# Optimization experiments

Hardware: AMD Instinct MI355X
Metric: run time of the kernel (lower is better)

The kernel has to match this reference:

```python
import jax, jax.numpy as jnp
import numpy as np

EPS = 1e-8


def setup_inputs() -> dict:
    key = jax.random.key(0)
    ks = jax.random.split(key, 10)
    B, Cin, H, W = 16, 256, 64, 64
    D, C = 128, 32
    return {
        "f_curr": jax.random.normal(ks[0], (B, Cin, H, W), jnp.float32),
        "mu_prior": jax.random.normal(ks[1], (B, D, C), jnp.float32),
        "log_sigma_prior": jax.random.normal(ks[2], (B, D, C), jnp.float32),
        "pi_prior": jax.random.uniform(ks[3], (B, C), jnp.float32),
        "mu_post": jax.random.normal(ks[4], (B, D), jnp.float32),
        "log_sigma_post": jax.random.normal(ks[5], (B, D), jnp.float32),
        "noise_cluster": jax.random.normal(ks[6], (B, D), jnp.float32),
        "noise_z": jax.random.normal(ks[7], (B, D), jnp.float32),
        "proj_W": jax.random.normal(ks[8], (Cin, Cin + D), jnp.float32) * 0.02,
        "proj_b": jax.random.normal(ks[9], (Cin,), jnp.float32) * 0.02,
    }


def reference(f_curr, mu_prior, log_sigma_prior, pi_prior, mu_post,
              log_sigma_post, noise_cluster, noise_z, proj_W, proj_b):
    sg = jax.lax.stop_gradient

    # ---- _cluster_sampler (all stats detached in the original) ----
    mu_p, ls_p = sg(mu_post), sg(log_sigma_post)          # [B, D]
    mu_pr, ls_pr = sg(mu_prior), sg(log_sigma_prior)      # [B, D, C]
    z_post = mu_p + jnp.exp(ls_p) * noise_cluster          # Normal(mu, exp(ls)).sample()
    sigma_pr = jnp.exp(ls_pr)
    # Normal log_prob of z_post[:, :, None] under each cluster -> [B, D, C]
    log_probs = (-ls_pr - 0.5 * jnp.log(2.0 * jnp.pi)
                 - (z_post[:, :, None] - mu_pr) ** 2 / (2.0 * sigma_pr ** 2))
    log_prob_c = jnp.sum(log_probs, axis=1)                # [B, C]
    pi_post = jax.nn.softmax(log_prob_c, axis=1)           # [B, C]

    # ---- z_c = Normal(mu_post, exp(ls)+eps).sample()  (no grad: .sample()) ----
    z_c = sg(mu_post + (jnp.exp(log_sigma_post) + EPS) * noise_z)  # [B, D]

    # ---- _f_combine: concat + 1x1 conv, computed as split matmuls ----
    Cin = f_curr.shape[1]
    Wf, Wz = proj_W[:, :Cin], proj_W[:, Cin:]              # [Cin,Cin], [Cin,D]
    bias = jnp.einsum('bd,od->bo', z_c, Wz) + proj_b       # spatially-constant part
    f_out = jnp.einsum('bchw,oc->bohw', f_curr, Wf) + bias[:, :, None, None]

    # ---- _kld ----
    mu_post_e = mu_post[:, :, None]                        # [B, D, 1]
    ls_post_e = log_sigma_post[:, :, None]
    sigma_prior = jnp.exp(log_sigma_prior)
    sigma_post = jnp.exp(ls_post_e)
    kl_g = (log_sigma_prior - ls_post_e
            + (sigma_post ** 2 + (mu_post_e - mu_prior) ** 2)
            / (2.0 * sigma_prior ** 2 + EPS) - 0.5)
    kl_g = jnp.sum(kl_g, axis=1)                           # [B, C]
    kl_g_weighted = jnp.sum(pi_post * kl_g, axis=1)        # [B]
    kl_cat = jnp.sum(pi_post * (jnp.log(pi_post + EPS) - jnp.log(pi_prior + EPS)), axis=1)  # [B]
    kl_std = jnp.sum(-ls_post_e + 0.5 * (jnp.exp(2.0 * ls_post_e) + mu_post_e ** 2) - 0.5,
                     axis=1)                               # [B, 1]
    # NOTE: original torch code broadcasts [B] + [B,1] -> [B,B] before mean; replicated here.
    kld = jnp.mean((kl_g_weighted + kl_cat) + kl_std)

    return f_out, kld
```

## Files before the change

kernel.cpp:

```cpp
#include <hip/hip_runtime.h>
#include <math.h>

#define EPS_F 1e-8f

typedef __attribute__((ext_vector_type(8))) short bf16x8;
typedef __attribute__((ext_vector_type(4))) float f32x4;

__device__ inline short f2bf(float f) {
    union { float f; unsigned u; } v; v.f = f;
    unsigned r = (v.u + 0x7fffu + ((v.u >> 16) & 1u)) >> 16;
    return (short)r;
}

__global__ __launch_bounds__(256) void prelim_kernel(
    const float* __restrict__ mu_prior,
    const float* __restrict__ ls_prior,
    const float* __restrict__ pi_prior,
    const float* __restrict__ mu_post,
    const float* __restrict__ ls_post,
    const float* __restrict__ noise_c,
    const float* __restrict__ noise_z,
    const float* __restrict__ projW,
    const float* __restrict__ projb,
    float* __restrict__ ws_bias,
    float* __restrict__ kld_out)
{
    const int b = blockIdx.x;
    const int t = threadIdx.x;

    __shared__ float s_zpost[128];
    __shared__ float s_zc[128];
    __shared__ float s_mu[128];
    __shared__ float s_e2[128];
    __shared__ float s_lsp[128];
    __shared__ float s_kstd[128];
    __shared__ float s_p1[8][32];
    __shared__ float s_p2[8][32];

    if (t < 128) {
        const float mu = mu_post[b * 128 + t];
        const float ls = ls_post[b * 128 + t];
        const float el = __expf(ls);
        s_zpost[t] = mu + el * noise_c[b * 128 + t];
        s_zc[t]    = mu + (el + EPS_F) * noise_z[b * 128 + t];
        s_mu[t]    = mu;
        s_e2[t]    = el * el;
        s_lsp[t]   = ls;
        s_kstd[t]  = -ls + 0.5f * (el * el + mu * mu) - 0.5f;
    }
    __syncthreads();

    {
        const int c = t & 31;
        const int g = t >> 5;
        const float* mpB = mu_prior + b * 4096;
        const float* lpB = ls_prior + b * 4096;
        float lp = 0.f, kg = 0.f;
#pragma unroll 4
        for (int j = 0; j < 16; ++j) {
            const int d = g * 16 + j;
            const float mpr  = mpB[d * 32 + c];
            const float lpr  = lpB[d * 32 + c];
            const float inv2 = 0.5f * __expf(-2.f * lpr);
            const float zd   = s_zpost[d] - mpr;
            lp += -lpr - 0.91893853320467274f - zd * zd * inv2;
            const float dm   = s_mu[d] - mpr;
            const float e2pr = __expf(2.f * lpr);
            kg += lpr - s_lsp[d]
                + (s_e2[d] + dm * dm) * __builtin_amdgcn_rcpf(2.f * e2pr + EPS_F)
                - 0.5f;
        }
        s_p1[g][c] = lp;
        s_p2[g][c] = kg;
    }
    __syncthreads();

    if (t < 64) {
        const int c = t & 31;
        float lp = 0.f, kg = 0.f;
#pragma unroll
        for (int g = 0; g < 8; ++g) { lp += s_p1[g][c]; kg += s_p2[g][c]; }
        float ks = s_kstd[c] + s_kstd[c + 32] + s_kstd[c + 64] + s_kstd[c + 96];
        const float pp = pi_prior[b * 32 + c];

        float m = lp;
#pragma unroll
        for (int o = 16; o; o >>= 1) m = fmaxf(m, __shfl_xor(m, o, 32));
        const float e = __expf(lp - m);
        float den = e;
#pragma unroll
        for (int o = 16; o; o >>= 1) den += __shfl_xor(den, o, 32);
        const float pi = e * __builtin_amdgcn_rcpf(den);
        float tot = pi * kg + pi * (__logf(pi + EPS_F) - __logf(pp + EPS_F));
#pragma unroll
        for (int o = 16; o; o >>= 1) tot += __shfl_xor(tot, o, 32);
#pragma unroll
        for (int o = 16; o; o >>= 1) ks += __shfl_xor(ks, o, 32);
        if (t == 0) atomicAdd(kld_out, (tot + ks) * 0.0625f);
    }

    {
        const int o = t;
        const float4* wrow = (const float4*)(projW + o * 384 + 256);
        float sum = projb[o];
#pragma unroll 8
        for (int j = 0; j < 32; ++j) {
            const float4 w = wrow[j];
            sum += s_zc[4 * j + 0] * w.x + s_zc[4 * j + 1] * w.y +
                   s_zc[4 * j + 2] * w.z + s_zc[4 * j + 3] * w.w;
        }
        ws_bias[b * 256 + o] = sum;
    }
}

__global__ __launch_bounds__(512, 2) void gemm_kernel(
    const float* __restrict__ F,
    const float* __restrict__ W,
    const float* __restrict__ bias,
    float* __restrict__ O)
{
    const int nT = blockIdx.x;
    const int b  = blockIdx.y;

    __shared__ short A_lds[4][256][8];
    __shared__ short B_lds[4][128][8];
    __shared__ float s_bias[256];

    const int tid  = threadIdx.x;
    const int lane = tid & 63;
    const int wave = tid >> 6;
    const int wm = wave & 3;
    const int wn = wave >> 2;

    const float* Fb = F + (size_t)b * 256 * 4096 + (size_t)nT * 128;

    const int sbn = tid & 127;
    const int sbk = tid >> 7;
    const int sao = tid >> 1;
    const int sak = (tid & 1) * 2;

    if (tid < 256) s_bias[tid] = bias[b * 256 + tid];

    const float* bptr = Fb + (size_t)(sbk * 8) * 4096 + sbn;
    const float* aptr = W + sao * 384 + sak * 8;

    float fb[8];
    float4 fa0, fa1, fa2, fa3;

#pragma unroll
    for (int i = 0; i < 8; ++i) fb[i] = bptr[(size_t)i * 4096];
    fa0 = *(const float4*)(aptr);
    fa1 = *(const float4*)(aptr + 4);
    fa2 = *(const float4*)(aptr + 8);
    fa3 = *(const float4*)(aptr + 12);

    f32x4 acc[4][4];
#pragma unroll
    for (int i = 0; i < 4; ++i)
#pragma unroll
        for (int j = 0; j < 4; ++j) acc[i][j] = (f32x4){0.f, 0.f, 0.f, 0.f};

    const int kg = lane >> 4;
    const int lm = lane & 15;

    for (int kc = 0; kc < 8; ++kc) {
        bf16x8 vb, va0, va1;
#pragma unroll
        for (int i = 0; i < 8; ++i) vb[i] = f2bf(fb[i]);
        va0[0] = f2bf(fa0.x); va0[1] = f2bf(fa0.y); va0[2] = f2bf(fa0.z); va0[3] = f2bf(fa0.w);
        va0[4] = f2bf(fa1.x); va0[5] = f2bf(fa1.y); va0[6] = f2bf(fa1.z); va0[7] = f2bf(fa1.w);
        va1[0] = f2bf(fa2.x); va1[1] = f2bf(fa2.y); va1[2] = f2bf(fa2.z); va1[3] = f2bf(fa2.w);
        va1[4] = f2bf(fa3.x); va1[5] = f2bf(fa3.y); va1[6] = f2bf(fa3.z); va1[7] = f2bf(fa3.w);

        __syncthreads();
        *(bf16x8*)&B_lds[sbk][sbn][0]     = vb;
        *(bf16x8*)&A_lds[sak][sao][0]     = va0;
        *(bf16x8*)&A_lds[sak + 1][sao][0] = va1;
        __syncthreads();

        if (kc < 7) {
            const float* bp = bptr + (size_t)(kc + 1) * 32 * 4096;
#pragma unroll
            for (int i = 0; i < 8; ++i) fb[i] = bp[(size_t)i * 4096];
            const float* ap = aptr + (kc + 1) * 32;
            fa0 = *(const float4*)(ap);
            fa1 = *(const float4*)(ap + 4);
            fa2 = *(const float4*)(ap + 8);
            fa3 = *(const float4*)(ap + 12);
        }

        bf16x8 aF[4], bF[4];
#pragma unroll
        for (int mt = 0; mt < 4; ++mt)
            aF[mt] = *(const bf16x8*)&A_lds[kg][wm * 64 + mt * 16 + lm][0];
#pragma unroll
        for (int nt = 0; nt < 4; ++nt)
            bF[nt] = *(const bf16x8*)&B_lds[kg][wn * 64 + nt * 16 + lm][0];

#pragma unroll
        for (int mt = 0; mt < 4; ++mt)
#pragma unroll
            for (int nt = 0; nt < 4; ++nt)
                acc[mt][nt] = __builtin_amdgcn_mfma_f32_16x16x32_bf16(
                    aF[mt], bF[nt], acc[mt][nt], 0, 0, 0);
    }

    float* Ob = O + (size_t)b * 256 * 4096;
    const int rbase = wm * 64 + (lane >> 4) * 4;
    const int cbase = nT * 128 + wn * 64 + (lane & 15);
#pragma unroll
    for (int mt = 0; mt < 4; ++mt) {
#pragma unroll
        for (int r = 0; r < 4; ++r) {
            const int row = rbase + mt * 16 + r;
            const float bb = s_bias[row];
            float* orow = Ob + (size_t)row * 4096 + cbase;
#pragma unroll
            for (int nt = 0; nt < 4; ++nt)
                orow[nt * 16] = acc[mt][nt][r] + bb;
        }
    }
}

extern "C" void kernel_launch(void* const* d_in, const int* in_sizes, int n_in,
                              void* d_out, int out_size, void* d_ws, size_t ws_size,
                              hipStream_t stream) {
    const float* f_curr   = (const float*)d_in[0];
    const float* mu_prior = (const float*)d_in[1];
    const float* ls_prior = (const float*)d_in[2];
    const float* pi_prior = (const float*)d_in[3];
    const float* mu_post  = (const float*)d_in[4];
    const float* ls_post  = (const float*)d_in[5];
    const float* noise_c  = (const float*)d_in[6];
    const float* noise_z  = (const float*)d_in[7];
    const float* projW    = (const float*)d_in[8];
    const float* projb    = (const float*)d_in[9];

    float* out = (float*)d_out;
    float* ws  = (float*)d_ws;
    float* ws_bias = ws;

    float* kld_out = out + 16777216;
    hipMemsetAsync(kld_out, 0, sizeof(float), stream);

    prelim_kernel<<<16, 256, 0, stream>>>(mu_prior, ls_prior, pi_prior, mu_post,
                                          ls_post, noise_c, noise_z, projW, projb,
                                          ws_bias, kld_out);
    gemm_kernel<<<dim3(32, 16), 512, 0, stream>>>(f_curr, projW, ws_bias, out);
}
```

Baseline: 156.3 us.

## Split GEMM output channels across two blocks with 256-thread tiles

The GEMM grid gains an output-channel tile dimension, so each block computes a 128x128 output tile with 4 waves instead of a 256x128 tile with 8 waves. This doubles the block count (1024 blocks) to improve occupancy and load balance across CUs. Each thread now stages 16 F values per k-chunk. The cost is that every F tile is read twice from global memory, once per output-channel half, and per-block staging work rises.

```diff
diff --git a/kernel.cpp b/kernel.cpp
--- a/kernel.cpp
+++ b/kernel.cpp
@@ -113,42 +113,43 @@
     }
 }
 
-__global__ __launch_bounds__(512, 2) void gemm_kernel(
+__global__ __launch_bounds__(256) void gemm_kernel(
     const float* __restrict__ F,
     const float* __restrict__ W,
     const float* __restrict__ bias,
     float* __restrict__ O)
 {
     const int nT = blockIdx.x;
-    const int b  = blockIdx.y;
-
-    __shared__ short A_lds[4][256][8];
+    const int oT = blockIdx.y;
+    const int b  = blockIdx.z;
+
+    __shared__ short A_lds[4][128][8];
     __shared__ short B_lds[4][128][8];
-    __shared__ float s_bias[256];
+    __shared__ float s_bias[128];
 
     const int tid  = threadIdx.x;
     const int lane = tid & 63;
     const int wave = tid >> 6;
-    const int wm = wave & 3;
-    const int wn = wave >> 2;
+    const int wm = wave & 1;
+    const int wn = wave >> 1;
 
     const float* Fb = F + (size_t)b * 256 * 4096 + (size_t)nT * 128;
 
-    const int sbn = tid & 127;
-    const int sbk = tid >> 7;
-    const int sao = tid >> 1;
-    const int sak = (tid & 1) * 2;
-
-    if (tid < 256) s_bias[tid] = bias[b * 256 + tid];
-
-    const float* bptr = Fb + (size_t)(sbk * 8) * 4096 + sbn;
-    const float* aptr = W + sao * 384 + sak * 8;
-
-    float fb[8];
+    const int sbn  = tid & 127;
+    const int sbkg = (tid >> 7) * 2;
+    const int sao  = tid >> 1;
+    const int sakg = (tid & 1) * 2;
+
+    if (tid < 128) s_bias[tid] = bias[b * 256 + oT * 128 + tid];
+
+    const float* bptr = Fb + (size_t)(sbkg * 8) * 4096 + sbn;
+    const float* aptr = W + (size_t)(oT * 128 + sao) * 384 + sakg * 8;
+
+    float fb[16];
     float4 fa0, fa1, fa2, fa3;
 
 #pragma unroll
-    for (int i = 0; i < 8; ++i) fb[i] = bptr[(size_t)i * 4096];
+    for (int i = 0; i < 16; ++i) fb[i] = bptr[(size_t)i * 4096];
     fa0 = *(const float4*)(aptr);
     fa1 = *(const float4*)(aptr + 4);
     fa2 = *(const float4*)(aptr + 8);
@@ -164,24 +165,27 @@
     const int lm = lane & 15;
 
     for (int kc = 0; kc < 8; ++kc) {
-        bf16x8 vb, va0, va1;
-#pragma unroll
-        for (int i = 0; i < 8; ++i) vb[i] = f2bf(fb[i]);
+        bf16x8 vb0, vb1, va0, va1;
+#pragma unroll
+        for (int i = 0; i < 8; ++i) vb0[i] = f2bf(fb[i]);
+#pragma unroll
+        for (int i = 0; i < 8; ++i) vb1[i] = f2bf(fb[8 + i]);
         va0[0] = f2bf(fa0.x); va0[1] = f2bf(fa0.y); va0[2] = f2bf(fa0.z); va0[3] = f2bf(fa0.w);
         va0[4] = f2bf(fa1.x); va0[5] = f2bf(fa1.y); va0[6] = f2bf(fa1.z); va0[7] = f2bf(fa1.w);
         va1[0] = f2bf(fa2.x); va1[1] = f2bf(fa2.y); va1[2] = f2bf(fa2.z); va1[3] = f2bf(fa2.w);
         va1[4] = f2bf(fa3.x); va1[5] = f2bf(fa3.y); va1[6] = f2bf(fa3.z); va1[7] = f2bf(fa3.w);
 
         __syncthreads();
-        *(bf16x8*)&B_lds[sbk][sbn][0]     = vb;
-        *(bf16x8*)&A_lds[sak][sao][0]     = va0;
-        *(bf16x8*)&A_lds[sak + 1][sao][0] = va1;
+        *(bf16x8*)&B_lds[sbkg][sbn][0]      = vb0;
+        *(bf16x8*)&B_lds[sbkg + 1][sbn][0]  = vb1;
+        *(bf16x8*)&A_lds[sakg][sao][0]      = va0;
+        *(bf16x8*)&A_lds[sakg + 1][sao][0]  = va1;
         __syncthreads();
 
         if (kc < 7) {
             const float* bp = bptr + (size_t)(kc + 1) * 32 * 4096;
 #pragma unroll
-            for (int i = 0; i < 8; ++i) fb[i] = bp[(size_t)i * 4096];
+            for (int i = 0; i < 16; ++i) fb[i] = bp[(size_t)i * 4096];
             const float* ap = aptr + (kc + 1) * 32;
             fa0 = *(const float4*)(ap);
             fa1 = *(const float4*)(ap + 4);
@@ -205,9 +209,9 @@
                     aF[mt], bF[nt], acc[mt][nt], 0, 0, 0);
     }
 
-    float* Ob = O + (size_t)b * 256 * 4096;
+    float* Ob = O + (size_t)b * 256 * 4096 + (size_t)oT * 128 * 4096;
     const int rbase = wm * 64 + (lane >> 4) * 4;
-    const int cbase = nT * 128 + wn * 64 + (lane & 15);
+    const int cbase = nT * 128 + wn * 64 + lm;
 #pragma unroll
     for (int mt = 0; mt < 4; ++mt) {
 #pragma unroll
@@ -246,5 +250,5 @@
     prelim_kernel<<<16, 256, 0, stream>>>(mu_prior, ls_prior, pi_prior, mu_post,
                                           ls_post, noise_c, noise_z, projW, projb,
                                           ws_bias, kld_out);
-    gemm_kernel<<<dim3(32, 16), 512, 0, stream>>>(f_curr, projW, ws_bias, out);
-}
+    gemm_kernel<<<dim3(32, 2, 16), 256, 0, stream>>>(f_curr, projW, ws_bias, out);
+}
```

Result: no change. 158.0 us (+1.1%).
